# Kernel tuning notes

Measured on AMD Instinct MI355X. Metric: run time of the kernel, lower is better.

Reference implementation:

```python
import jax, jax.numpy as jnp
import numpy as np

B, S, C_IN, D, H = 16, 1024, 1280, 512, 8
HD = D // H  # head dim = 64
EPS = 1e-5


def _rope(x):
    # x: [b, h, s, d]; half-split rotation as in the torch module
    d = x.shape[-1]
    half = d // 2
    s = x.shape[2]
    inv_freq = 1.0 / (10000.0 ** (jnp.arange(0, d, 2, dtype=jnp.float32) / d))  # [half]
    ang = jnp.arange(s, dtype=jnp.float32)[:, None] * inv_freq[None, :]  # [s, half]
    sin, cos = jnp.sin(ang), jnp.cos(ang)  # broadcast over [b, h]
    x1, x2 = x[..., :half], x[..., half:]
    return jnp.concatenate([x1 * cos - x2 * sin, x1 * sin + x2 * cos], axis=-1)


def _ln(x, g, b):
    mu = jnp.mean(x, axis=-1, keepdims=True)
    var = jnp.mean((x - mu) ** 2, axis=-1, keepdims=True)
    return (x - mu) * jax.lax.rsqrt(var + EPS) * g + b


def setup_inputs() -> dict:
    key = jax.random.key(0)
    ks = jax.random.split(key, 12)
    def lin(k, fan_in, fan_out):
        lim = 1.0 / np.sqrt(fan_in)
        return jax.random.uniform(k, (fan_in, fan_out), jnp.float32, -lim, lim)
    return {
        "x": jax.random.normal(ks[0], (B, S, C_IN), jnp.float32),
        "w_in": lin(ks[1], C_IN, D), "b_in": jnp.zeros((D,), jnp.float32),
        "w_qkv": lin(ks[2], D, 3 * D), "b_qkv": jnp.zeros((3 * D,), jnp.float32),
        "w_out": lin(ks[3], D, D), "b_out": jnp.zeros((D,), jnp.float32),
        "w_ffn1": lin(ks[4], D, 4 * D), "b_ffn1": jnp.zeros((4 * D,), jnp.float32),
        "w_ffn2": lin(ks[5], 4 * D, D), "b_ffn2": jnp.zeros((D,), jnp.float32),
        "g1": jnp.ones((D,), jnp.float32), "bn1": jnp.zeros((D,), jnp.float32),
        "g2": jnp.ones((D,), jnp.float32), "bn2": jnp.zeros((D,), jnp.float32),
    }


def reference(x, w_in, b_in, w_qkv, b_qkv, w_out, b_out,
              w_ffn1, b_ffn1, w_ffn2, b_ffn2, g1, bn1, g2, bn2):
    h = x @ w_in + b_in  # [b, s, D]
    qkv = (h @ w_qkv + b_qkv).reshape(B, S, 3, H, HD)
    q, k, v = (jnp.transpose(qkv[:, :, i], (0, 2, 1, 3)) for i in range(3))  # [b, h, s, d]
    q, k = _rope(q), _rope(k)
    scores = jnp.einsum('bhqd,bhkd->bhqk', q, k) / np.sqrt(HD)
    attn = jax.nn.softmax(scores, axis=-1)
    o = jnp.einsum('bhqk,bhkd->bhqd', attn, v)
    o = jnp.transpose(o, (0, 2, 1, 3)).reshape(B, S, D)
    o = o @ w_out + b_out
    h = _ln(h + o, g1, bn1)
    ffn = jax.nn.relu(h @ w_ffn1 + b_ffn1) @ w_ffn2 + b_ffn2
    return _ln(h + ffn, g2, bn2)
```

## Files before the change

### kernel.cpp

```cpp
#include <hip/hip_runtime.h>
#include <hip/hip_bf16.h>
#include <math.h>

#define B_   16
#define S_   1024
#define CIN  1280
#define D_   512
#define H_   8
#define HD_  64
#define NROW (B_ * S_)

typedef __bf16 bf16;
typedef float  f32x2  __attribute__((ext_vector_type(2)));
typedef float  f32x4  __attribute__((ext_vector_type(4)));
typedef bf16   bf16x4 __attribute__((ext_vector_type(4)));
typedef bf16   bf16x8 __attribute__((ext_vector_type(8)));

__device__ __forceinline__ void gload_lds16(const bf16* g, bf16* l) {
    __builtin_amdgcn_global_load_lds(
        (const __attribute__((address_space(1))) void*)g,
        (__attribute__((address_space(3))) void*)l, 16, 0, 0);
}

#define SBAR()   __builtin_amdgcn_s_barrier()
#define SCHED0() __builtin_amdgcn_sched_barrier(0)
#define VMCNT8() asm volatile("s_waitcnt vmcnt(8)" ::: "memory")
#define VMCNT2() asm volatile("s_waitcnt vmcnt(2)" ::: "memory")
#define VMCNT0() asm volatile("s_waitcnt vmcnt(0)" ::: "memory")

__global__ void cvt_kernel(const float* __restrict__ in, bf16* __restrict__ out, int n4)
{
    int i = blockIdx.x * blockDim.x + threadIdx.x;
    if (i >= n4) return;
    f32x4 v = *(const f32x4*)(in + (size_t)i * 4);
    bf16x4 o;
    o[0] = (bf16)v[0]; o[1] = (bf16)v[1]; o[2] = (bf16)v[2]; o[3] = (bf16)v[3];
    *(bf16x4*)(out + (size_t)i * 4) = o;
}

__global__ __launch_bounds__(256)
void tr_cvt_kernel(const float* __restrict__ in, bf16* __restrict__ out, int R, int C)
{
    __shared__ float T[32][33];
    const int r0 = blockIdx.y << 5, c0 = blockIdx.x << 5;
    const int t  = threadIdx.x;
    {
        int lr = t >> 3, lc = (t & 7) << 2;
        f32x4 v = *(const f32x4*)(in + (size_t)(r0 + lr) * C + c0 + lc);
        T[lr][lc] = v[0]; T[lr][lc + 1] = v[1]; T[lr][lc + 2] = v[2]; T[lr][lc + 3] = v[3];
    }
    __syncthreads();
    {
        int oc = t >> 3, orr = (t & 7) << 2;
        bf16x4 o;
        o[0] = (bf16)T[orr][oc];     o[1] = (bf16)T[orr + 1][oc];
        o[2] = (bf16)T[orr + 2][oc]; o[3] = (bf16)T[orr + 3][oc];
        *(bf16x4*)(out + (size_t)(c0 + oc) * R + r0 + orr) = o;
    }
}

__global__ void cs_kernel(float* __restrict__ cs)
{
    int idx = blockIdx.x * 256 + threadIdx.x;
    int s = idx >> 5, i = idx & 31;
    float freq = exp2f(-(float)i * (13.287712379549449f / 32.f));
    float sn, c;
    sincosf((float)s * freq, &sn, &c);
    cs[(size_t)idx * 2]     = c;
    cs[(size_t)idx * 2 + 1] = sn;
}

#define ASZ1 (128 * 64)

template<int EPI, bool RELU, bool RES, bool OUTF, bool OUTB>
__global__ __launch_bounds__(256, 2)
void gemm128_kernel(const bf16* __restrict__ A, const bf16* __restrict__ Wt,
                    const float* __restrict__ bias, const bf16* __restrict__ res,
                    float* __restrict__ outf, bf16* __restrict__ outb,
                    const float* __restrict__ cs, bf16* __restrict__ vt,
                    int M, int N, int K)
{
    __shared__ bf16 lds[4 * ASZ1];

    const int tid  = threadIdx.x;
    const int lane = tid & 63;
    const int wid  = tid >> 6;

    const int perX = (M >> 7) >> 3;
    const int lin  = blockIdx.x;
    const int idx  = lin >> 3;
    const int my   = (lin & 7) * perX + (idx & (perX - 1));
    const int nx   = idx / perX;
    const int m0   = my << 7, n0 = nx << 7;

    const int sRow = lane >> 3;
    const int sK   = ((lane & 7) ^ sRow) << 3;

    const int r2  = wid >> 1;
    const int c2  = wid & 1;
    const int cc  = lane & 15;
    const int g   = (lane >> 4) & 3;
    const int swz = (cc & 7) << 4;

    f32x4 acc[4][4] = {};

    auto stage = [&](int t, int b) {
        const bf16* gA = A  + (size_t)m0 * K + t * 64;
        const bf16* gB = Wt + (size_t)n0 * K + t * 64;
        bf16* lA = lds + b * ASZ1;
        bf16* lB = lds + 2 * ASZ1 + b * ASZ1;
        #pragma unroll
        for (int v = 0; v < 4; ++v) {
            const int ch = v * 4 + wid;
            gload_lds16(gA + (size_t)(ch * 8 + sRow) * K + sK, lA + ch * 512);
            gload_lds16(gB + (size_t)(ch * 8 + sRow) * K + sK, lB + ch * 512);
        }
    };

    const int T = K >> 6;
    stage(0, 0);
    stage(1, 1);
    VMCNT8();
    SCHED0();
    SBAR();

    for (int t = 0; t < T; ++t) {
        const int b = t & 1;
        const char* lA = (const char*)(lds + b * ASZ1);
        const char* lB = (const char*)(lds + 2 * ASZ1 + b * ASZ1);

        #pragma unroll
        for (int ks = 0; ks < 2; ++ks) {
            bf16x8 af[4], bfr[4];
            #pragma unroll
            for (int i = 0; i < 4; ++i) {
                const int row = r2 * 64 + i * 16 + cc;
                af[i] = *(const bf16x8*)(lA + row * 128 + ((ks * 64 + g * 16) ^ swz));
            }
            #pragma unroll
            for (int j = 0; j < 4; ++j) {
                const int row = c2 * 64 + j * 16 + cc;
                bfr[j] = *(const bf16x8*)(lB + row * 128 + ((ks * 64 + g * 16) ^ swz));
            }
            __builtin_amdgcn_s_setprio(1);
            #pragma unroll
            for (int i = 0; i < 4; ++i)
                #pragma unroll
                for (int j = 0; j < 4; ++j)
                    acc[i][j] = __builtin_amdgcn_mfma_f32_16x16x32_bf16(af[i], bfr[j], acc[i][j], 0, 0, 0);
            __builtin_amdgcn_s_setprio(0);
        }
        SCHED0();
        SBAR();
        if (t + 2 < T) {
            stage(t + 2, b);
            VMCNT8();
        } else if (t + 1 < T) {
            VMCNT0();
        }
        if (t + 1 < T) { SCHED0(); SBAR(); }
    }

    const int rq = g << 2;
    if constexpr (EPI == 1) {
        const int colb = c2 * 64;
        if (nx < 8) {
            float bj[4];
            #pragma unroll
            for (int j = 0; j < 4; ++j) bj[j] = bias[n0 + colb + j * 16 + cc];
            #pragma unroll
            for (int i = 0; i < 4; ++i) {
                #pragma unroll
                for (int r = 0; r < 4; ++r) {
                    const int gm = m0 + r2 * 64 + i * 16 + rq + r;
                    const int s  = gm & (S_ - 1);
                    #pragma unroll
                    for (int jp = 0; jp < 2; ++jp) {
                        const int d = jp * 16 + cc;
                        f32x2 csv = *(const f32x2*)(cs + ((size_t)s * 32 + d) * 2);
                        float x1 = acc[i][jp][r]     + bj[jp];
                        float x2 = acc[i][jp + 2][r] + bj[jp + 2];
                        const size_t o1 = (size_t)gm * N + n0 + colb + d;
                        outb[o1]      = (bf16)(x1 * csv[0] - x2 * csv[1]);
                        outb[o1 + 32] = (bf16)(x1 * csv[1] + x2 * csv[0]);
                    }
                }
            }
        } else {
            const int col0 = n0 + colb;
            const int hw = (col0 >> 6) & 7;
            const int bb = m0 >> 10;
            bf16* vbase = vt + (size_t)(bb * 8 + hw) * (HD_ * S_);
            const int sb0 = (m0 & (S_ - 1)) + r2 * 64 + rq;
            #pragma unroll
            for (int i = 0; i < 4; ++i) {
                #pragma unroll
                for (int j = 0; j < 4; ++j) {
                    const int d = j * 16 + cc;
                    const float bv = bias[col0 + d];
                    bf16x4 pk;
                    #pragma unroll
                    for (int r = 0; r < 4; ++r) pk[r] = (bf16)(acc[i][j][r] + bv);
                    *(bf16x4*)(vbase + (size_t)d * S_ + sb0 + i * 16) = pk;
                }
            }
        }
    } else {
        #pragma unroll
        for (int i = 0; i < 4; ++i) {
            #pragma unroll
            for (int j = 0; j < 4; ++j) {
                const int gn = n0 + c2 * 64 + j * 16 + cc;
                const float bv = bias[gn];
                #pragma unroll
                for (int r = 0; r < 4; ++r) {
                    const int gm = m0 + r2 * 64 + i * 16 + rq + r;
                    float v = acc[i][j][r] + bv;
                    if (RES)  v += (float)res[(size_t)gm * N + gn];
                    if (RELU) v = fmaxf(v, 0.f);
                    if (OUTF) outf[(size_t)gm * N + gn] = v;
                    if (OUTB) outb[(size_t)gm * N + gn] = (bf16)v;
                }
            }
        }
    }
    (void)cs; (void)vt;
}

#define PST 72

__global__ __launch_bounds__(512)
void attn_kernel(const bf16* __restrict__ qkv, const bf16* __restrict__ vtg,
                 bf16* __restrict__ o)
{
    __shared__ bf16 Ks[2][4096];
    __shared__ bf16 Vs[2][4096];
    __shared__ bf16 Ps[8][16 * PST];

    const int bh  = blockIdx.x;
    const int b   = bh >> 3;
    const int h   = bh & 7;
    const int q0  = blockIdx.y << 7;
    const int tid = threadIdx.x;
    const int lane = tid & 63;
    const int w    = tid >> 6;
    const int c    = lane & 15;
    const int g    = lane >> 4;
    const int swz  = (c & 7) << 4;

    const size_t rs = 3 * D_;
    const bf16* qb = qkv + (size_t)b * S_ * rs + h * HD_;
    const bf16* kb = qb + D_;
    const bf16* vt = vtg + (size_t)bh * HD_ * S_;

    const int sRow = tid >> 3;
    const int sOff = ((tid & 7) ^ (sRow & 7)) << 3;

    bf16x8 qf[2];
    {
        const bf16* qrow = qb + (size_t)(q0 + w * 16 + c) * rs + g * 8;
        qf[0] = *(const bf16x8*)(qrow);
        qf[1] = *(const bf16x8*)(qrow + 32);
    }
    SCHED0();

    bf16x8 vones;
    {
        bf16 one = (bf16)(c == 0 ? 1.f : 0.f);
        #pragma unroll
        for (int u = 0; u < 8; ++u) vones[u] = one;
    }

    auto stage = [&](int t, int buf) {
        gload_lds16(kb + (size_t)(t * 64 + sRow) * rs + sOff, &Ks[buf][0] + (size_t)tid * 8);
        gload_lds16(vt + (size_t)sRow * S_ + t * 64 + sOff,   &Vs[buf][0] + (size_t)tid * 8);
    };

    f32x4 oa[4] = {};
    f32x4 oa5 = {};
    float m_r = -3.0e38f;
    const float CE  = 0.18033688011112042f;
    const float THR = 44.3614195558365f;

    stage(0, 0);
    stage(1, 1);
    VMCNT2();
    SCHED0();
    SBAR();

    for (int t = 0; t < 16; ++t) {
        const int buf = t & 1;
        const char* kB = (const char*)Ks[buf];
        const char* vB = (const char*)Vs[buf];

        f32x4 sa[4] = {};
        __builtin_amdgcn_s_setprio(1);
        #pragma unroll
        for (int ch = 0; ch < 2; ++ch)
            #pragma unroll
            for (int ks = 0; ks < 4; ++ks) {
                bf16x8 kf = *(const bf16x8*)(kB + (ks * 16 + c) * 128 + ((ch * 64 + g * 16) ^ swz));
                sa[ks] = __builtin_amdgcn_mfma_f32_16x16x32_bf16(kf, qf[ch], sa[ks], 0, 0, 0);
            }
        __builtin_amdgcn_s_setprio(0);

        float pmax = -3.0e38f;
        #pragma unroll
        for (int ks = 0; ks < 4; ++ks)
            pmax = fmaxf(pmax, fmaxf(fmaxf(sa[ks][0], sa[ks][1]), fmaxf(sa[ks][2], sa[ks][3])));
        pmax = fmaxf(pmax, __shfl_xor(pmax, 16, 64));
        pmax = fmaxf(pmax, __shfl_xor(pmax, 32, 64));

        if (!__all(pmax - m_r <= THR)) {
            float mnew = fmaxf(m_r, pmax);
            float sc = __builtin_amdgcn_exp2f((m_r - mnew) * CE);
            #pragma unroll
            for (int r = 0; r < 4; ++r) {
                float scr = __shfl(sc, g * 4 + r, 64);
                #pragma unroll
                for (int j = 0; j < 4; ++j) oa[j][r] *= scr;
                oa5[r] *= scr;
            }
            m_r = mnew;
        }

        const float nmCE = -m_r * CE;
        #pragma unroll
        for (int ks = 0; ks < 4; ++ks) {
            bf16x4 pb;
            #pragma unroll
            for (int r = 0; r < 4; ++r)
                pb[r] = (bf16)__builtin_amdgcn_exp2f(__builtin_fmaf(sa[ks][r], CE, nmCE));
            *(bf16x4*)&Ps[w][c * PST + ks * 16 + g * 4] = pb;
        }

        __builtin_amdgcn_s_setprio(1);
        #pragma unroll
        for (int ch = 0; ch < 2; ++ch) {
            bf16x8 pa = *(const bf16x8*)&Ps[w][c * PST + ch * 32 + g * 8];
            #pragma unroll
            for (int j = 0; j < 4; ++j) {
                bf16x8 vf = *(const bf16x8*)(vB + (j * 16 + c) * 128 + ((ch * 64 + g * 16) ^ swz));
                oa[j] = __builtin_amdgcn_mfma_f32_16x16x32_bf16(pa, vf, oa[j], 0, 0, 0);
            }
            oa5 = __builtin_amdgcn_mfma_f32_16x16x32_bf16(pa, vones, oa5, 0, 0, 0);
        }
        __builtin_amdgcn_s_setprio(0);

        SCHED0();
        SBAR();
        if (t + 2 < 16) {
            stage(t + 2, buf);
            VMCNT2();
        } else if (t + 1 < 16) {
            VMCNT0();
        }
        if (t + 1 < 16) { SCHED0(); SBAR(); }
    }

    float linv[4];
    #pragma unroll
    for (int r = 0; r < 4; ++r)
        linv[r] = 1.f / __shfl(oa5[r], lane & 48, 64);
    #pragma unroll
    for (int j = 0; j < 4; ++j)
        #pragma unroll
        for (int r = 0; r < 4; ++r) {
            int q = q0 + w * 16 + g * 4 + r;
            o[((size_t)(b * S_) + q) * D_ + h * HD_ + j * 16 + c] = (bf16)(oa[j][r] * linv[r]);
        }
}

template<bool OUTF, bool OUTB>
__global__ __launch_bounds__(256)
void ln_kernel(const float* __restrict__ in, const float* __restrict__ g,
               const float* __restrict__ be, float* __restrict__ outf,
               bf16* __restrict__ outb)
{
    const int row  = (blockIdx.x << 2) + (threadIdx.x >> 6);
    const int lane = threadIdx.x & 63;
    const float* p = in + (size_t)row * D_;
    f32x4 a  = *(const f32x4*)(p + lane * 4);
    f32x4 b2 = *(const f32x4*)(p + 256 + lane * 4);
    float s  = a[0] + a[1] + a[2] + a[3] + b2[0] + b2[1] + b2[2] + b2[3];
    float s2 = a[0]*a[0] + a[1]*a[1] + a[2]*a[2] + a[3]*a[3]
             + b2[0]*b2[0] + b2[1]*b2[1] + b2[2]*b2[2] + b2[3]*b2[3];
    #pragma unroll
    for (int off = 32; off; off >>= 1) {
        s  += __shfl_xor(s,  off, 64);
        s2 += __shfl_xor(s2, off, 64);
    }
    const float mean = s * (1.f / 512.f);
    const float var  = s2 * (1.f / 512.f) - mean * mean;
    const float rstd = rsqrtf(var + 1e-5f);

    f32x4 g0 = *(const f32x4*)(g + lane * 4);
    f32x4 g1 = *(const f32x4*)(g + 256 + lane * 4);
    f32x4 e0 = *(const f32x4*)(be + lane * 4);
    f32x4 e1 = *(const f32x4*)(be + 256 + lane * 4);
    f32x4 o0, o1;
    #pragma unroll
    for (int u = 0; u < 4; u++) {
        o0[u] = (a[u]  - mean) * rstd * g0[u] + e0[u];
        o1[u] = (b2[u] - mean) * rstd * g1[u] + e1[u];
    }
    if (OUTF) {
        float* of = outf + (size_t)row * D_;
        *(f32x4*)(of + lane * 4)       = o0;
        *(f32x4*)(of + 256 + lane * 4) = o1;
    }
    if (OUTB) {
        bf16x4 c0, c1;
        #pragma unroll
        for (int u = 0; u < 4; u++) { c0[u] = (bf16)o0[u]; c1[u] = (bf16)o1[u]; }
        bf16* ob = outb + (size_t)row * D_;
        *(bf16x4*)(ob + lane * 4)       = c0;
        *(bf16x4*)(ob + 256 + lane * 4) = c1;
    }
}

extern "C" void kernel_launch(void* const* d_in, const int* in_sizes, int n_in,
                              void* d_out, int out_size, void* d_ws, size_t ws_size,
                              hipStream_t stream)
{
    const float* x      = (const float*)d_in[0];
    const float* w_in   = (const float*)d_in[1];
    const float* b_in   = (const float*)d_in[2];
    const float* w_qkv  = (const float*)d_in[3];
    const float* b_qkv  = (const float*)d_in[4];
    const float* w_out  = (const float*)d_in[5];
    const float* b_out  = (const float*)d_in[6];
    const float* w_ffn1 = (const float*)d_in[7];
    const float* b_ffn1 = (const float*)d_in[8];
    const float* w_ffn2 = (const float*)d_in[9];
    const float* b_ffn2 = (const float*)d_in[10];
    const float* g1     = (const float*)d_in[11];
    const float* bn1    = (const float*)d_in[12];
    const float* g2     = (const float*)d_in[13];
    const float* bn2    = (const float*)d_in[14];

    char* ws = (char*)d_ws;
    constexpr size_t OFF_XB   = 0;
    constexpr size_t OFF_WIN  = OFF_XB   + 41943040ull;
    constexpr size_t OFF_WQKV = OFF_WIN  + 1310720ull;
    constexpr size_t OFF_WOUT = OFF_WQKV + 1572864ull;
    constexpr size_t OFF_WF1  = OFF_WOUT + 524288ull;
    constexpr size_t OFF_WF2  = OFF_WF1  + 2097152ull;
    constexpr size_t OFF_CS   = OFF_WF2  + 2097152ull;
    constexpr size_t OFF_HB   = OFF_CS   + 33554432ull;
    constexpr size_t OFF_QKV  = OFF_HB   + 16777216ull;
    constexpr size_t OFF_OB   = OFF_QKV  + 50331648ull;
    constexpr size_t OFF_VT   = OFF_OB   + 16777216ull;
    constexpr size_t OFF_H2B  = OFF_VT   + 33554432ull;
    constexpr size_t OFF_F1   = OFF_H2B  + 16777216ull;
    constexpr size_t OFF_T1   = OFF_XB;
    constexpr size_t OFF_T2   = OFF_QKV;

    bf16*  x_b    = (bf16*)(ws + OFF_XB);
    bf16*  win_t  = (bf16*)(ws + OFF_WIN);
    bf16*  wqkv_t = (bf16*)(ws + OFF_WQKV);
    bf16*  wout_t = (bf16*)(ws + OFF_WOUT);
    bf16*  wf1_t  = (bf16*)(ws + OFF_WF1);
    bf16*  wf2_t  = (bf16*)(ws + OFF_WF2);
    float* cs_t   = (float*)(ws + OFF_CS);
    bf16*  h_b    = (bf16*)(ws + OFF_HB);
    bf16*  qkv_b  = (bf16*)(ws + OFF_QKV);
    bf16*  o_b    = (bf16*)(ws + OFF_OB);
    bf16*  vt_g   = (bf16*)(ws + OFF_VT);
    bf16*  h2_b   = (bf16*)(ws + OFF_H2B);
    bf16*  f1_b   = (bf16*)(ws + OFF_F1);
    float* t1_f   = (float*)(ws + OFF_T1);
    float* t2_f   = (float*)(ws + OFF_T2);

    {
        int n4 = NROW * CIN / 4;
        cvt_kernel<<<(n4 + 255) / 256, 256, 0, stream>>>(x, x_b, n4);
    }
    tr_cvt_kernel<<<dim3(512/32, 1280/32), 256, 0, stream>>>(w_in,   win_t,  1280, 512);
    tr_cvt_kernel<<<dim3(1536/32, 512/32), 256, 0, stream>>>(w_qkv,  wqkv_t, 512, 1536);
    tr_cvt_kernel<<<dim3(512/32,  512/32), 256, 0, stream>>>(w_out,  wout_t, 512, 512);
    tr_cvt_kernel<<<dim3(2048/32, 512/32), 256, 0, stream>>>(w_ffn1, wf1_t,  512, 2048);
    tr_cvt_kernel<<<dim3(512/32, 2048/32), 256, 0, stream>>>(w_ffn2, wf2_t,  2048, 512);
    cs_kernel<<<128, 256, 0, stream>>>(cs_t);

    gemm128_kernel<0,false,false,false,true><<<(NROW/128) * (D_/128), 256, 0, stream>>>(
        x_b, win_t, b_in, nullptr, nullptr, h_b, nullptr, nullptr, NROW, D_, CIN);
    gemm128_kernel<1,false,false,false,true><<<(NROW/128) * (3*D_/128), 256, 0, stream>>>(
        h_b, wqkv_t, b_qkv, nullptr, nullptr, qkv_b, cs_t, vt_g, NROW, 3*D_, D_);
    attn_kernel<<<dim3(B_*H_, S_/128), 512, 0, stream>>>(qkv_b, vt_g, o_b);
    gemm128_kernel<0,false,true,true,false><<<(NROW/128) * (D_/128), 256, 0, stream>>>(
        o_b, wout_t, b_out, h_b, t1_f, nullptr, nullptr, nullptr, NROW, D_, D_);
    ln_kernel<false,true><<<NROW/4, 256, 0, stream>>>(t1_f, g1, bn1, nullptr, h2_b);
    gemm128_kernel<0,true,false,false,true><<<(NROW/128) * (4*D_/128), 256, 0, stream>>>(
        h2_b, wf1_t, b_ffn1, nullptr, nullptr, f1_b, nullptr, nullptr, NROW, 4*D_, D_);
    gemm128_kernel<0,false,true,true,false><<<(NROW/128) * (D_/128), 256, 0, stream>>>(
        f1_b, wf2_t, b_ffn2, h2_b, t2_f, nullptr, nullptr, nullptr, NROW, D_, 4*D_);
    ln_kernel<true,false><<<NROW/4, 256, 0, stream>>>(t2_f, g2, bn2, (float*)d_out, nullptr);

    (void)in_sizes; (void)n_in; (void)out_size; (void)ws_size;
}
```

Measured before the change: 275.7 us.

## Merge prep kernels into one launch and load attention K/V directly from global

The seven preprocessing launches (x conversion, five weight transposes, rope table) are folded into a single prep kernel that picks its job from the block index, cutting launch overhead. Separately, the attention kernel no longer stages K and V tiles through double-buffered LDS with async global-to-LDS loads and barriers. Each wave now reads its K/V fragments straight from global memory and relies on cache, with launch bounds raised to allow more resident blocks. This removes barriers and frees LDS for occupancy, at the cost of redundant, less coalesced global reads that are no longer overlapped with compute.

New measurement: 484.9 us. 75.9% more time.

```diff
diff --git a/kernel.cpp b/kernel.cpp
--- a/kernel.cpp
+++ b/kernel.cpp
@@ -25,25 +25,14 @@
 #define SBAR()   __builtin_amdgcn_s_barrier()
 #define SCHED0() __builtin_amdgcn_sched_barrier(0)
 #define VMCNT8() asm volatile("s_waitcnt vmcnt(8)" ::: "memory")
-#define VMCNT2() asm volatile("s_waitcnt vmcnt(2)" ::: "memory")
 #define VMCNT0() asm volatile("s_waitcnt vmcnt(0)" ::: "memory")
 
-__global__ void cvt_kernel(const float* __restrict__ in, bf16* __restrict__ out, int n4)
-{
-    int i = blockIdx.x * blockDim.x + threadIdx.x;
-    if (i >= n4) return;
-    f32x4 v = *(const f32x4*)(in + (size_t)i * 4);
-    bf16x4 o;
-    o[0] = (bf16)v[0]; o[1] = (bf16)v[1]; o[2] = (bf16)v[2]; o[3] = (bf16)v[3];
-    *(bf16x4*)(out + (size_t)i * 4) = o;
-}
-
-__global__ __launch_bounds__(256)
-void tr_cvt_kernel(const float* __restrict__ in, bf16* __restrict__ out, int R, int C)
+__device__ __forceinline__ void tr_tile(const float* __restrict__ in,
+                                        bf16* __restrict__ out,
+                                        int R, int C, int cx, int ry, int t)
 {
     __shared__ float T[32][33];
-    const int r0 = blockIdx.y << 5, c0 = blockIdx.x << 5;
-    const int t  = threadIdx.x;
+    const int r0 = ry << 5, c0 = cx << 5;
     {
         int lr = t >> 3, lc = (t & 7) << 2;
         f32x4 v = *(const f32x4*)(in + (size_t)(r0 + lr) * C + c0 + lc);
@@ -59,16 +48,49 @@
     }
 }
 
-__global__ void cs_kernel(float* __restrict__ cs)
-{
-    int idx = blockIdx.x * 256 + threadIdx.x;
-    int s = idx >> 5, i = idx & 31;
-    float freq = exp2f(-(float)i * (13.287712379549449f / 32.f));
-    float sn, c;
-    sincosf((float)s * freq, &sn, &c);
-    cs[(size_t)idx * 2]     = c;
-    cs[(size_t)idx * 2 + 1] = sn;
-}
+#define NCVT (NROW * CIN / 4 / 256)
+
+__global__ __launch_bounds__(256)
+void prep_kernel(const float* __restrict__ x, bf16* __restrict__ x_b,
+                 const float* __restrict__ w_in,   bf16* __restrict__ win_t,
+                 const float* __restrict__ w_qkv,  bf16* __restrict__ wqkv_t,
+                 const float* __restrict__ w_out,  bf16* __restrict__ wout_t,
+                 const float* __restrict__ w_ffn1, bf16* __restrict__ wf1_t,
+                 const float* __restrict__ w_ffn2, bf16* __restrict__ wf2_t,
+                 float* __restrict__ cs)
+{
+    const int t   = threadIdx.x;
+    int bid = blockIdx.x;
+    if (bid < NCVT) {
+        int i = bid * 256 + t;
+        f32x4 v = *(const f32x4*)(x + (size_t)i * 4);
+        bf16x4 o;
+        o[0] = (bf16)v[0]; o[1] = (bf16)v[1]; o[2] = (bf16)v[2]; o[3] = (bf16)v[3];
+        *(bf16x4*)(x_b + (size_t)i * 4) = o;
+        return;
+    }
+    bid -= NCVT;
+    if (bid < 640)  { tr_tile(w_in,   win_t,  1280, 512,  bid % 16, bid / 16, t); return; }
+    bid -= 640;
+    if (bid < 768)  { tr_tile(w_qkv,  wqkv_t, 512,  1536, bid % 48, bid / 48, t); return; }
+    bid -= 768;
+    if (bid < 256)  { tr_tile(w_out,  wout_t, 512,  512,  bid % 16, bid / 16, t); return; }
+    bid -= 256;
+    if (bid < 1024) { tr_tile(w_ffn1, wf1_t,  512,  2048, bid % 64, bid / 64, t); return; }
+    bid -= 1024;
+    if (bid < 1024) { tr_tile(w_ffn2, wf2_t,  2048, 512,  bid % 16, bid / 16, t); return; }
+    bid -= 1024;
+    {
+        int idx = bid * 256 + t;
+        int s = idx >> 5, i = idx & 31;
+        float freq = exp2f(-(float)i * (13.287712379549449f / 32.f));
+        float sn, c;
+        sincosf((float)s * freq, &sn, &c);
+        cs[(size_t)idx * 2]     = c;
+        cs[(size_t)idx * 2 + 1] = sn;
+    }
+}
+#define NPREP (NCVT + 640 + 768 + 256 + 1024 + 1024 + 128)
 
 #define ASZ1 (128 * 64)
 
@@ -229,12 +251,10 @@
 
 #define PST 72
 
-__global__ __launch_bounds__(512)
+__global__ __launch_bounds__(512, 6)
 void attn_kernel(const bf16* __restrict__ qkv, const bf16* __restrict__ vtg,
                  bf16* __restrict__ o)
 {
-    __shared__ bf16 Ks[2][4096];
-    __shared__ bf16 Vs[2][4096];
     __shared__ bf16 Ps[8][16 * PST];
 
     const int bh  = blockIdx.x;
@@ -246,15 +266,11 @@
     const int w    = tid >> 6;
     const int c    = lane & 15;
     const int g    = lane >> 4;
-    const int swz  = (c & 7) << 4;
 
     const size_t rs = 3 * D_;
     const bf16* qb = qkv + (size_t)b * S_ * rs + h * HD_;
     const bf16* kb = qb + D_;
     const bf16* vt = vtg + (size_t)bh * HD_ * S_;
-
-    const int sRow = tid >> 3;
-    const int sOff = ((tid & 7) ^ (sRow & 7)) << 3;
 
     bf16x8 qf[2];
     {
@@ -262,7 +278,6 @@
         qf[0] = *(const bf16x8*)(qrow);
         qf[1] = *(const bf16x8*)(qrow + 32);
     }
-    SCHED0();
 
     bf16x8 vones;
     {
@@ -270,11 +285,6 @@
         #pragma unroll
         for (int u = 0; u < 8; ++u) vones[u] = one;
     }
-
-    auto stage = [&](int t, int buf) {
-        gload_lds16(kb + (size_t)(t * 64 + sRow) * rs + sOff, &Ks[buf][0] + (size_t)tid * 8);
-        gload_lds16(vt + (size_t)sRow * S_ + t * 64 + sOff,   &Vs[buf][0] + (size_t)tid * 8);
-    };
 
     f32x4 oa[4] = {};
     f32x4 oa5 = {};
@@ -282,24 +292,15 @@
     const float CE  = 0.18033688011112042f;
     const float THR = 44.3614195558365f;
 
-    stage(0, 0);
-    stage(1, 1);
-    VMCNT2();
-    SCHED0();
-    SBAR();
-
     for (int t = 0; t < 16; ++t) {
-        const int buf = t & 1;
-        const char* kB = (const char*)Ks[buf];
-        const char* vB = (const char*)Vs[buf];
-
         f32x4 sa[4] = {};
+        const bf16* kt = kb + (size_t)t * 64 * rs;
         __builtin_amdgcn_s_setprio(1);
         #pragma unroll
         for (int ch = 0; ch < 2; ++ch)
             #pragma unroll
             for (int ks = 0; ks < 4; ++ks) {
-                bf16x8 kf = *(const bf16x8*)(kB + (ks * 16 + c) * 128 + ((ch * 64 + g * 16) ^ swz));
+                bf16x8 kf = *(const bf16x8*)(kt + (size_t)(ks * 16 + c) * rs + ch * 32 + g * 8);
                 sa[ks] = __builtin_amdgcn_mfma_f32_16x16x32_bf16(kf, qf[ch], sa[ks], 0, 0, 0);
             }
         __builtin_amdgcn_s_setprio(0);
@@ -334,28 +335,19 @@
             *(bf16x4*)&Ps[w][c * PST + ks * 16 + g * 4] = pb;
         }
 
+        const bf16* vtt = vt + t * 64;
         __builtin_amdgcn_s_setprio(1);
         #pragma unroll
         for (int ch = 0; ch < 2; ++ch) {
             bf16x8 pa = *(const bf16x8*)&Ps[w][c * PST + ch * 32 + g * 8];
             #pragma unroll
             for (int j = 0; j < 4; ++j) {
-                bf16x8 vf = *(const bf16x8*)(vB + (j * 16 + c) * 128 + ((ch * 64 + g * 16) ^ swz));
+                bf16x8 vf = *(const bf16x8*)(vtt + (size_t)(j * 16 + c) * S_ + ch * 32 + g * 8);
                 oa[j] = __builtin_amdgcn_mfma_f32_16x16x32_bf16(pa, vf, oa[j], 0, 0, 0);
             }
             oa5 = __builtin_amdgcn_mfma_f32_16x16x32_bf16(pa, vones, oa5, 0, 0, 0);
         }
         __builtin_amdgcn_s_setprio(0);
-
-        SCHED0();
-        SBAR();
-        if (t + 2 < 16) {
-            stage(t + 2, buf);
-            VMCNT2();
-        } else if (t + 1 < 16) {
-            VMCNT0();
-        }
-        if (t + 1 < 16) { SCHED0(); SBAR(); }
     }
 
     float linv[4];
@@ -472,16 +464,9 @@
     float* t1_f   = (float*)(ws + OFF_T1);
     float* t2_f   = (float*)(ws + OFF_T2);
 
-    {
-        int n4 = NROW * CIN / 4;
-        cvt_kernel<<<(n4 + 255) / 256, 256, 0, stream>>>(x, x_b, n4);
-    }
-    tr_cvt_kernel<<<dim3(512/32, 1280/32), 256, 0, stream>>>(w_in,   win_t,  1280, 512);
-    tr_cvt_kernel<<<dim3(1536/32, 512/32), 256, 0, stream>>>(w_qkv,  wqkv_t, 512, 1536);
-    tr_cvt_kernel<<<dim3(512/32,  512/32), 256, 0, stream>>>(w_out,  wout_t, 512, 512);
-    tr_cvt_kernel<<<dim3(2048/32, 512/32), 256, 0, stream>>>(w_ffn1, wf1_t,  512, 2048);
-    tr_cvt_kernel<<<dim3(512/32, 2048/32), 256, 0, stream>>>(w_ffn2, wf2_t,  2048, 512);
-    cs_kernel<<<128, 256, 0, stream>>>(cs_t);
+    prep_kernel<<<NPREP, 256, 0, stream>>>(x, x_b, w_in, win_t, w_qkv, wqkv_t,
+                                           w_out, wout_t, w_ffn1, wf1_t,
+                                           w_ffn2, wf2_t, cs_t);
 
     gemm128_kernel<0,false,false,false,true><<<(NROW/128) * (D_/128), 256, 0, stream>>>(
         x_b, win_t, b_in, nullptr, nullptr, h_b, nullptr, nullptr, NROW, D_, CIN);
```
